# Kernel optimization log

Hardware: AMD Instinct MI355X
Metric: run time of the kernel (lower is better)

The kernel has to match this reference:

```python
import jax, jax.numpy as jnp
import numpy as np

NUM_HEADS = 16
HEAD_DIM = 64  # hidden 1024 / 16 heads


def setup_inputs() -> dict:
    key = jax.random.key(0)
    ks = jax.random.split(key, 4)
    B, S, D = 2, 2048, 1024
    scale = 1.0 / np.sqrt(D)
    return {
        "hidden_states": jax.random.normal(ks[0], (B, S, D), jnp.float32),
        "Wq": jax.random.normal(ks[1], (D, D), jnp.float32) * scale,
        "bq": jnp.zeros((D,), jnp.float32),
        "Wk": jax.random.normal(ks[2], (D, D), jnp.float32) * scale,
        "bk": jnp.zeros((D,), jnp.float32),
        "Wv": jax.random.normal(ks[3], (D, D), jnp.float32) * scale,
        "bv": jnp.zeros((D,), jnp.float32),
    }


def _split_heads(x):
    B, S, D = x.shape
    return x.reshape(B, S, NUM_HEADS, HEAD_DIM).transpose(0, 2, 1, 3)  # [B,H,S,dh]


def reference(hidden_states, Wq, bq, Wk, bk, Wv, bv):
    q = _split_heads(hidden_states @ Wq + bq)
    k = _split_heads(hidden_states @ Wk + bk)
    v = _split_heads(hidden_states @ Wv + bv)
    scores = jnp.einsum("bhqd,bhkd->bhqk", q, k) / jnp.sqrt(
        jnp.asarray(HEAD_DIM, hidden_states.dtype))
    probs = jax.nn.softmax(scores, axis=-1)  # dropout is identity in eval mode
    ctx = jnp.einsum("bhqk,bhkd->bhqd", probs, v)
    B, H, S, dh = ctx.shape
    return ctx.transpose(0, 2, 1, 3).reshape(B, S, H * dh)
```

## Files before the change

### kernel.cpp

```cpp
#include <hip/hip_runtime.h>
#include <hip/hip_bf16.h>


typedef __attribute__((ext_vector_type(8))) short bf16x8;
typedef __attribute__((ext_vector_type(4))) float f32x4;
typedef __attribute__((ext_vector_type(4))) int int4v;

#define MFMA16(A, B, C) __builtin_amdgcn_mfma_f32_16x16x32_bf16((A), (B), (C), 0, 0, 0)

#if __has_builtin(__builtin_amdgcn_exp2f)
#define EXP2(x) __builtin_amdgcn_exp2f(x)
#else
#define EXP2(x) exp2f(x)
#endif

static __device__ __forceinline__ unsigned short f2bf(float f) {
    union { float f; unsigned int u; } v;
    v.f = f;
    unsigned int u = v.u;
    u += ((u >> 16) & 1u) + 0x7FFFu;
    return (unsigned short)(u >> 16);
}

static __device__ __forceinline__ void gload_lds16(const void* g, void* l) {
    __builtin_amdgcn_global_load_lds(
        (const __attribute__((address_space(1))) void*)g,
        (__attribute__((address_space(3))) void*)l, 16, 0, 0);
}

__global__ __launch_bounds__(256) void cast_hs(const float* __restrict__ in,
                                               unsigned short* __restrict__ out) {
    const size_t i = ((size_t)blockIdx.x * 256 + threadIdx.x) * 8;
    float4 a0 = *reinterpret_cast<const float4*>(in + i);
    float4 a1 = *reinterpret_cast<const float4*>(in + i + 4);
    unsigned short t[8];
    t[0] = f2bf(a0.x); t[1] = f2bf(a0.y); t[2] = f2bf(a0.z); t[3] = f2bf(a0.w);
    t[4] = f2bf(a1.x); t[5] = f2bf(a1.y); t[6] = f2bf(a1.z); t[7] = f2bf(a1.w);
    *reinterpret_cast<int4v*>(out + i) = *reinterpret_cast<int4v*>(t);
}

__global__ __launch_bounds__(256) void transpose_cast_w(
    const float* __restrict__ W0, const float* __restrict__ W1,
    const float* __restrict__ W2, unsigned short* __restrict__ Wt) {
    __shared__ float Ts[64][65];
    const float* W = (blockIdx.z == 0) ? W0 : (blockIdx.z == 1) ? W1 : W2;
    unsigned short* O = Wt + (size_t)blockIdx.z * 1048576;

    const int t  = threadIdx.x;
    const int k0 = blockIdx.y * 64;
    const int n0 = blockIdx.x * 64;

    {
        const int kr = t >> 2, nc = (t & 3) * 16;
        const float* p = W + (size_t)(k0 + kr) * 1024 + n0 + nc;
        float4 r0 = *reinterpret_cast<const float4*>(p);
        float4 r1 = *reinterpret_cast<const float4*>(p + 4);
        float4 r2 = *reinterpret_cast<const float4*>(p + 8);
        float4 r3 = *reinterpret_cast<const float4*>(p + 12);
        float* d = &Ts[kr][nc];
        d[0]=r0.x; d[1]=r0.y; d[2]=r0.z; d[3]=r0.w;
        d[4]=r1.x; d[5]=r1.y; d[6]=r1.z; d[7]=r1.w;
        d[8]=r2.x; d[9]=r2.y; d[10]=r2.z; d[11]=r2.w;
        d[12]=r3.x; d[13]=r3.y; d[14]=r3.z; d[15]=r3.w;
    }
    __syncthreads();
    {
        const int nr = t >> 2, kc = (t & 3) * 16;
        unsigned short tmp[16];
#pragma unroll
        for (int i = 0; i < 16; i++) tmp[i] = f2bf(Ts[kc + i][nr]);
        unsigned short* d = O + (size_t)(n0 + nr) * 1024 + k0 + kc;
        *reinterpret_cast<int4v*>(d)     = *reinterpret_cast<int4v*>(&tmp[0]);
        *reinterpret_cast<int4v*>(d + 8) = *reinterpret_cast<int4v*>(&tmp[8]);
    }
}

__global__ __launch_bounds__(256) void qkv_gemm_dma(
    const unsigned short* __restrict__ hsb,
    const unsigned short* __restrict__ Wt,
    const float* __restrict__ b0, const float* __restrict__ b1,
    const float* __restrict__ b2,
    unsigned short* __restrict__ Qo,
    unsigned short* __restrict__ Ko,
    unsigned short* __restrict__ Vto)
{
    __shared__ unsigned short As[128][32];
    __shared__ unsigned short Bs[128][32];

    const int z = blockIdx.z;
    const unsigned short* W = Wt + (size_t)z * 1048576;
    const float* bias = (z == 0) ? b0 : (z == 1) ? b1 : b2;

    const int tid  = threadIdx.x;
    const int lane = tid & 63;
    const int w    = tid >> 6;
    const int l15  = lane & 15;
    const int quad = lane >> 4;
    const int m0   = blockIdx.y * 128;
    const int n0   = blockIdx.x * 128;
    const int wm   = (w >> 1) * 64;
    const int wn   = (w & 1) * 64;

    const int drow = lane >> 2;
    const int dcol = (lane & 3) * 8;

    f32x4 acc[4][4];
#pragma unroll
    for (int i = 0; i < 4; i++)
#pragma unroll
        for (int j = 0; j < 4; j++)
            acc[i][j] = (f32x4){0.f, 0.f, 0.f, 0.f};

    for (int k0 = 0; k0 < 1024; k0 += 32) {
        __syncthreads();
#pragma unroll
        for (int p = 0; p < 2; p++) {
            const int s = w * 2 + p;
            gload_lds16(hsb + (size_t)(m0 + s * 16 + drow) * 1024 + k0 + dcol,
                        &As[s * 16][0]);
            gload_lds16(W   + (size_t)(n0 + s * 16 + drow) * 1024 + k0 + dcol,
                        &Bs[s * 16][0]);
        }
        __syncthreads();

        bf16x8 af[4], bfr[4];
#pragma unroll
        for (int i = 0; i < 4; i++)
            af[i] = *reinterpret_cast<const bf16x8*>(&As[wm + i * 16 + l15][quad * 8]);
#pragma unroll
        for (int j = 0; j < 4; j++)
            bfr[j] = *reinterpret_cast<const bf16x8*>(&Bs[wn + j * 16 + l15][quad * 8]);
#pragma unroll
        for (int i = 0; i < 4; i++)
#pragma unroll
            for (int j = 0; j < 4; j++)
                acc[i][j] = MFMA16(af[i], bfr[j], acc[i][j]);
    }

    if (z == 0) {
        const float qs = 0.18033688f;
#pragma unroll
        for (int i = 0; i < 4; i++) {
            const int mbase = m0 + wm + i * 16 + quad * 4;
#pragma unroll
            for (int j = 0; j < 4; j++) {
                const int n = n0 + wn + j * 16 + l15;
                const int h = n >> 6, d = n & 63;
                const float bn = bias[n];
#pragma unroll
                for (int r = 0; r < 4; r++) {
                    const int mm = mbase + r;
                    const int b = mm >> 11, s = mm & 2047;
                    Qo[(((size_t)(b * 16 + h) * 2048 + s) * 64) + d] =
                        f2bf((acc[i][j][r] + bn) * qs);
                }
            }
        }
    } else if (z == 1) {
#pragma unroll
        for (int i = 0; i < 4; i++) {
            const int mbase = m0 + wm + i * 16 + quad * 4;
#pragma unroll
            for (int j = 0; j < 4; j++) {
                const int n = n0 + wn + j * 16 + l15;
                const int h = n >> 6, d = n & 63;
                const float bn = bias[n];
#pragma unroll
                for (int r = 0; r < 4; r++) {
                    const int mm = mbase + r;
                    const int b = mm >> 11, s = mm & 2047;
                    const int dsw = ((((d >> 3) ^ (s & 7)) & 7) << 3) | (d & 7);
                    Ko[(((size_t)(b * 16 + h) * 2048 + s) * 64) + dsw] =
                        f2bf(acc[i][j][r] + bn);
                }
            }
        }
    } else {
#pragma unroll
        for (int i = 0; i < 4; i++) {
            const int mbase = m0 + wm + i * 16 + quad * 4;
            const int b = mbase >> 11, s0 = mbase & 2047;
#pragma unroll
            for (int j = 0; j < 4; j++) {
                const int n = n0 + wn + j * 16 + l15;
                const int h = n >> 6, d = n & 63;
                const float bn = bias[n];
                ushort4 v4;
                v4.x = f2bf(acc[i][j][0] + bn);
                v4.y = f2bf(acc[i][j][1] + bn);
                v4.z = f2bf(acc[i][j][2] + bn);
                v4.w = f2bf(acc[i][j][3] + bn);
                const int cs  = (s0 & 63) >> 3;
                const int ssw = (s0 & ~63) | (((cs ^ (d & 7)) & 7) << 3) | (s0 & 7);
                *reinterpret_cast<ushort4*>(
                    Vto + ((size_t)(b * 16 + h) * 64 + d) * 2048 + ssw) = v4;
            }
        }
    }
}

__global__ __launch_bounds__(512) void attn3(
    const unsigned short* __restrict__ Qg,
    const unsigned short* __restrict__ Kg,
    const unsigned short* __restrict__ Vtg,
    float* __restrict__ out)
{
    __shared__ unsigned short Ks[2][64][64];
    __shared__ unsigned short Vs[2][64][64];
    __shared__ unsigned short Ps[8][16][66];

    const int tid  = threadIdx.x;
    const int lane = tid & 63;
    const int w    = tid >> 6;
    const int l15  = lane & 15;
    const int quad = lane >> 4;

    const int q0 = blockIdx.x * 128;
    const int h  = blockIdx.y;
    const int b  = blockIdx.z;
    const size_t base = (size_t)(b * 16 + h) * 2048 * 64;
    const unsigned short* Qh  = Qg  + base;
    const unsigned short* Kh  = Kg  + base;
    const unsigned short* Vth = Vtg + base;

    const int drow = lane >> 3;
    const int dcol = (lane & 7) * 8;

    bf16x8 qf[2];
#pragma unroll
    for (int ks = 0; ks < 2; ks++)
        qf[ks] = *reinterpret_cast<const bf16x8*>(
            Qh + (size_t)(q0 + w * 16 + l15) * 64 + ks * 32 + quad * 8);

    f32x4 o[4];
#pragma unroll
    for (int t = 0; t < 4; t++) o[t] = (f32x4){0.f, 0.f, 0.f, 0.f};
    float rsum[4] = {0.f, 0.f, 0.f, 0.f};

    const int c0 = (((quad + 0) ^ (l15 & 7)) & 7) * 8;
    const int c1 = (((quad + 4) ^ (l15 & 7)) & 7) * 8;

    gload_lds16(Kh  + (size_t)(w * 8 + drow) * 64 + dcol,   &Ks[0][w * 8][0]);
    gload_lds16(Vth + (size_t)(w * 8 + drow) * 2048 + dcol, &Vs[0][w * 8][0]);
    __syncthreads();

    int cur = 0;
    for (int kt = 0; kt < 32; kt++) {
        if (kt < 31) {
            const int kn = kt + 1;
            gload_lds16(Kh  + (size_t)kn * 4096 + (size_t)(w * 8 + drow) * 64 + dcol,
                        &Ks[cur ^ 1][w * 8][0]);
            gload_lds16(Vth + (size_t)(w * 8 + drow) * 2048 + kn * 64 + dcol,
                        &Vs[cur ^ 1][w * 8][0]);
        }

        const unsigned short (*Kc)[64] = Ks[cur];
        const unsigned short (*Vc)[64] = Vs[cur];

#pragma unroll
        for (int t = 0; t < 4; t++) {
            f32x4 sc = (f32x4){0.f, 0.f, 0.f, 0.f};
            {
                bf16x8 kf = *reinterpret_cast<const bf16x8*>(&Kc[t * 16 + l15][c0]);
                sc = MFMA16(qf[0], kf, sc);
            }
            {
                bf16x8 kf = *reinterpret_cast<const bf16x8*>(&Kc[t * 16 + l15][c1]);
                sc = MFMA16(qf[1], kf, sc);
            }
#pragma unroll
            for (int r = 0; r < 4; r++) {
                const float p = EXP2(sc[r]);
                rsum[r] += p;
                Ps[w][quad * 4 + r][t * 16 + l15] = f2bf(p);
            }
        }

        asm volatile("s_waitcnt lgkmcnt(0)" ::: "memory");
        __builtin_amdgcn_sched_barrier(0);

        bf16x8 pf[2];
#pragma unroll
        for (int ks = 0; ks < 2; ks++)
            pf[ks] = *reinterpret_cast<const bf16x8*>(&Ps[w][l15][ks * 32 + quad * 8]);

#pragma unroll
        for (int t = 0; t < 4; t++) {
            {
                bf16x8 vf = *reinterpret_cast<const bf16x8*>(&Vc[t * 16 + l15][c0]);
                o[t] = MFMA16(pf[0], vf, o[t]);
            }
            {
                bf16x8 vf = *reinterpret_cast<const bf16x8*>(&Vc[t * 16 + l15][c1]);
                o[t] = MFMA16(pf[1], vf, o[t]);
            }
        }

        __syncthreads();
        cur ^= 1;
    }

#pragma unroll
    for (int off = 1; off < 16; off <<= 1)
#pragma unroll
        for (int r = 0; r < 4; r++)
            rsum[r] += __shfl_xor(rsum[r], off, 64);

#pragma unroll
    for (int t = 0; t < 4; t++) {
#pragma unroll
        for (int r = 0; r < 4; r++) {
            const int q = q0 + w * 16 + quad * 4 + r;
            const size_t oidx = (((size_t)b * 2048 + q) * 16 + h) * 64 + t * 16 + l15;
            out[oidx] = o[t][r] / rsum[r];
        }
    }
}

__global__ void fill_sentinel(float* out, int n, float pat) {
    int i = blockIdx.x * blockDim.x + threadIdx.x;
    if (i < n) out[i] = pat;
}

extern "C" void kernel_launch(void* const* d_in, const int* in_sizes, int n_in,
                              void* d_out, int out_size, void* d_ws, size_t ws_size,
                              hipStream_t stream) {
    const size_t n_hs  = (size_t)4096 * 1024;
    const size_t n_w   = (size_t)1024 * 1024;
    const size_t n_qkv = n_hs;
    const size_t need = (n_hs + 3 * n_w + 3 * n_qkv) * sizeof(unsigned short);

    bool order_ok = (n_in == 7) &&
        in_sizes[0] == 4194304 &&
        in_sizes[1] == 1048576 && in_sizes[2] == 1024 &&
        in_sizes[3] == 1048576 && in_sizes[4] == 1024 &&
        in_sizes[5] == 1048576 && in_sizes[6] == 1024;
    if (!order_ok || out_size != 4194304) {
        fill_sentinel<<<(out_size + 255) / 256, 256, 0, stream>>>(
            (float*)d_out, out_size, 4.0f);
        return;
    }
    if (ws_size < need) {
        fill_sentinel<<<(out_size + 255) / 256, 256, 0, stream>>>(
            (float*)d_out, out_size, 2.0f);
        return;
    }

    const float* hs = (const float*)d_in[0];
    const float* Wq = (const float*)d_in[1];
    const float* bq = (const float*)d_in[2];
    const float* Wk = (const float*)d_in[3];
    const float* bk = (const float*)d_in[4];
    const float* Wv = (const float*)d_in[5];
    const float* bv = (const float*)d_in[6];

    unsigned short* hsb = (unsigned short*)d_ws;
    unsigned short* Wt  = hsb + n_hs;
    unsigned short* Q   = Wt + 3 * n_w;
    unsigned short* K   = Q + n_qkv;
    unsigned short* Vt  = K + n_qkv;

    cast_hs<<<2048, 256, 0, stream>>>(hs, hsb);
    transpose_cast_w<<<dim3(16, 16, 3), 256, 0, stream>>>(Wq, Wk, Wv, Wt);

    dim3 g1(8, 32, 3);
    qkv_gemm_dma<<<g1, dim3(256), 0, stream>>>(hsb, Wt, bq, bk, bv, Q, K, Vt);

    dim3 g2(16, 16, 2);
    attn3<<<g2, dim3(512), 0, stream>>>(Q, K, Vt, (float*)d_out);
}
```

Measured before the change: 196.9 us.

## Give each attention wave two query tiles and remap blocks onto a 1D grid

The attention kernel drops from 512 to 256 threads per block, and each wave now handles 32 query rows (two 16-row groups) instead of 16. Each K and V fragment read from LDS is reused across both groups, which halves LDS reads per MFMA. Blocks launch on a 1D grid whose index is remapped so that neighbouring blocks interleave batch-heads, which may help L2 locality and spread work across XCDs. In exchange each wave holds more registers, and there are half as many waves per block to hide latency.

```diff
diff --git a/kernel.cpp b/kernel.cpp
--- a/kernel.cpp
+++ b/kernel.cpp
@@ -199,7 +199,7 @@
     }
 }
 
-__global__ __launch_bounds__(512) void attn3(
+__global__ __launch_bounds__(256) void attn3(
     const unsigned short* __restrict__ Qg,
     const unsigned short* __restrict__ Kg,
     const unsigned short* __restrict__ Vtg,
@@ -207,7 +207,7 @@
 {
     __shared__ unsigned short Ks[2][64][64];
     __shared__ unsigned short Vs[2][64][64];
-    __shared__ unsigned short Ps[8][16][66];
+    __shared__ unsigned short Ps[4][32][68];
 
     const int tid  = threadIdx.x;
     const int lane = tid & 63;
@@ -215,43 +215,58 @@
     const int l15  = lane & 15;
     const int quad = lane >> 4;
 
-    const int q0 = blockIdx.x * 128;
-    const int h  = blockIdx.y;
-    const int b  = blockIdx.z;
-    const size_t base = (size_t)(b * 16 + h) * 2048 * 64;
+    const int lin = blockIdx.x;
+    const int qb  = (lin >> 3) & 15;
+    const int bh  = (lin & 7) | ((lin >> 7) << 3);
+    const int q0  = qb * 128;
+    const size_t base = (size_t)bh * 2048 * 64;
     const unsigned short* Qh  = Qg  + base;
     const unsigned short* Kh  = Kg  + base;
     const unsigned short* Vth = Vtg + base;
+    const int b = bh >> 4;
+    const int h = bh & 15;
 
     const int drow = lane >> 3;
     const int dcol = (lane & 7) * 8;
 
-    bf16x8 qf[2];
-#pragma unroll
-    for (int ks = 0; ks < 2; ks++)
-        qf[ks] = *reinterpret_cast<const bf16x8*>(
-            Qh + (size_t)(q0 + w * 16 + l15) * 64 + ks * 32 + quad * 8);
-
-    f32x4 o[4];
-#pragma unroll
-    for (int t = 0; t < 4; t++) o[t] = (f32x4){0.f, 0.f, 0.f, 0.f};
-    float rsum[4] = {0.f, 0.f, 0.f, 0.f};
+    bf16x8 qf[2][2];
+#pragma unroll
+    for (int g = 0; g < 2; g++)
+#pragma unroll
+        for (int ks = 0; ks < 2; ks++)
+            qf[g][ks] = *reinterpret_cast<const bf16x8*>(
+                Qh + (size_t)(q0 + w * 32 + g * 16 + l15) * 64 + ks * 32 + quad * 8);
+
+    f32x4 o[2][4];
+#pragma unroll
+    for (int g = 0; g < 2; g++)
+#pragma unroll
+        for (int t = 0; t < 4; t++) o[g][t] = (f32x4){0.f, 0.f, 0.f, 0.f};
+    float rsum[2][4] = {{0.f, 0.f, 0.f, 0.f}, {0.f, 0.f, 0.f, 0.f}};
 
     const int c0 = (((quad + 0) ^ (l15 & 7)) & 7) * 8;
     const int c1 = (((quad + 4) ^ (l15 & 7)) & 7) * 8;
 
-    gload_lds16(Kh  + (size_t)(w * 8 + drow) * 64 + dcol,   &Ks[0][w * 8][0]);
-    gload_lds16(Vth + (size_t)(w * 8 + drow) * 2048 + dcol, &Vs[0][w * 8][0]);
+#pragma unroll
+    for (int p = 0; p < 2; p++) {
+        const int s = w * 16 + p * 8;
+        gload_lds16(Kh  + (size_t)(s + drow) * 64 + dcol,   &Ks[0][s][0]);
+        gload_lds16(Vth + (size_t)(s + drow) * 2048 + dcol, &Vs[0][s][0]);
+    }
     __syncthreads();
 
     int cur = 0;
     for (int kt = 0; kt < 32; kt++) {
         if (kt < 31) {
             const int kn = kt + 1;
-            gload_lds16(Kh  + (size_t)kn * 4096 + (size_t)(w * 8 + drow) * 64 + dcol,
-                        &Ks[cur ^ 1][w * 8][0]);
-            gload_lds16(Vth + (size_t)(w * 8 + drow) * 2048 + kn * 64 + dcol,
-                        &Vs[cur ^ 1][w * 8][0]);
+#pragma unroll
+            for (int p = 0; p < 2; p++) {
+                const int s = w * 16 + p * 8;
+                gload_lds16(Kh  + (size_t)kn * 4096 + (size_t)(s + drow) * 64 + dcol,
+                            &Ks[cur ^ 1][s][0]);
+                gload_lds16(Vth + (size_t)(s + drow) * 2048 + kn * 64 + dcol,
+                            &Vs[cur ^ 1][s][0]);
+            }
         }
 
         const unsigned short (*Kc)[64] = Ks[cur];
@@ -259,40 +274,41 @@
 
 #pragma unroll
         for (int t = 0; t < 4; t++) {
-            f32x4 sc = (f32x4){0.f, 0.f, 0.f, 0.f};
-            {
-                bf16x8 kf = *reinterpret_cast<const bf16x8*>(&Kc[t * 16 + l15][c0]);
-                sc = MFMA16(qf[0], kf, sc);
-            }
-            {
-                bf16x8 kf = *reinterpret_cast<const bf16x8*>(&Kc[t * 16 + l15][c1]);
-                sc = MFMA16(qf[1], kf, sc);
-            }
-#pragma unroll
-            for (int r = 0; r < 4; r++) {
-                const float p = EXP2(sc[r]);
-                rsum[r] += p;
-                Ps[w][quad * 4 + r][t * 16 + l15] = f2bf(p);
+            bf16x8 kf0 = *reinterpret_cast<const bf16x8*>(&Kc[t * 16 + l15][c0]);
+            bf16x8 kf1 = *reinterpret_cast<const bf16x8*>(&Kc[t * 16 + l15][c1]);
+#pragma unroll
+            for (int g = 0; g < 2; g++) {
+                f32x4 sc = (f32x4){0.f, 0.f, 0.f, 0.f};
+                sc = MFMA16(qf[g][0], kf0, sc);
+                sc = MFMA16(qf[g][1], kf1, sc);
+#pragma unroll
+                for (int r = 0; r < 4; r++) {
+                    const float p = EXP2(sc[r]);
+                    rsum[g][r] += p;
+                    Ps[w][g * 16 + quad * 4 + r][t * 16 + l15] = f2bf(p);
+                }
             }
         }
 
         asm volatile("s_waitcnt lgkmcnt(0)" ::: "memory");
         __builtin_amdgcn_sched_barrier(0);
 
-        bf16x8 pf[2];
-#pragma unroll
-        for (int ks = 0; ks < 2; ks++)
-            pf[ks] = *reinterpret_cast<const bf16x8*>(&Ps[w][l15][ks * 32 + quad * 8]);
+        bf16x8 pf[2][2];
+#pragma unroll
+        for (int g = 0; g < 2; g++)
+#pragma unroll
+            for (int ks = 0; ks < 2; ks++)
+                pf[g][ks] = *reinterpret_cast<const bf16x8*>(
+                    &Ps[w][g * 16 + l15][ks * 32 + quad * 8]);
 
 #pragma unroll
         for (int t = 0; t < 4; t++) {
-            {
-                bf16x8 vf = *reinterpret_cast<const bf16x8*>(&Vc[t * 16 + l15][c0]);
-                o[t] = MFMA16(pf[0], vf, o[t]);
-            }
-            {
-                bf16x8 vf = *reinterpret_cast<const bf16x8*>(&Vc[t * 16 + l15][c1]);
-                o[t] = MFMA16(pf[1], vf, o[t]);
+            bf16x8 vf0 = *reinterpret_cast<const bf16x8*>(&Vc[t * 16 + l15][c0]);
+            bf16x8 vf1 = *reinterpret_cast<const bf16x8*>(&Vc[t * 16 + l15][c1]);
+#pragma unroll
+            for (int g = 0; g < 2; g++) {
+                o[g][t] = MFMA16(pf[g][0], vf0, o[g][t]);
+                o[g][t] = MFMA16(pf[g][1], vf1, o[g][t]);
             }
         }
 
@@ -303,18 +319,22 @@
 #pragma unroll
     for (int off = 1; off < 16; off <<= 1)
 #pragma unroll
-        for (int r = 0; r < 4; r++)
-            rsum[r] += __shfl_xor(rsum[r], off, 64);
-
-#pragma unroll
-    for (int t = 0; t < 4; t++) {
-#pragma unroll
-        for (int r = 0; r < 4; r++) {
-            const int q = q0 + w * 16 + quad * 4 + r;
-            const size_t oidx = (((size_t)b * 2048 + q) * 16 + h) * 64 + t * 16 + l15;
-            out[oidx] = o[t][r] / rsum[r];
-        }
-    }
+        for (int g = 0; g < 2; g++)
+#pragma unroll
+            for (int r = 0; r < 4; r++)
+                rsum[g][r] += __shfl_xor(rsum[g][r], off, 64);
+
+#pragma unroll
+    for (int g = 0; g < 2; g++)
+#pragma unroll
+        for (int t = 0; t < 4; t++)
+#pragma unroll
+            for (int r = 0; r < 4; r++) {
+                const int q = q0 + w * 32 + g * 16 + quad * 4 + r;
+                const size_t oidx =
+                    (((size_t)b * 2048 + q) * 16 + h) * 64 + t * 16 + l15;
+                out[oidx] = o[g][t][r] / rsum[g][r];
+            }
 }
 
 __global__ void fill_sentinel(float* out, int n, float pat) {
@@ -366,6 +386,5 @@
     dim3 g1(8, 32, 3);
     qkv_gemm_dma<<<g1, dim3(256), 0, stream>>>(hsb, Wt, bq, bk, bv, Q, K, Vt);
 
-    dim3 g2(16, 16, 2);
-    attn3<<<g2, dim3(512), 0, stream>>>(Q, K, Vt, (float*)d_out);
-}
+    attn3<<<dim3(512), dim3(256), 0, stream>>>(Q, K, Vt, (float*)d_out);
+}
```

New measurement: 193.6 us. No clear change (-1.7%).
